# Kernel tuning notes

Hardware: AMD Instinct MI355X
Metric: run time of the kernel (lower is better)

## Reference

```python
import jax, jax.numpy as jnp
import numpy as np
from jax import lax

TAU = 1.0  # registered buffer, default 1.0 -> Q_tau = +inf -> clamp is a no-op
EPS = 1e-5
SQRT2 = float(np.sqrt(2.0))

# sign with straight-through estimator (weights): grad = identity
@jax.custom_vjp
def sign_w(w):
    return jnp.sign(w)
def _sign_w_fwd(w):
    return jnp.sign(w), None
def _sign_w_bwd(_, g):
    return (g,)
sign_w.defvjp(_sign_w_fwd, _sign_w_bwd)

@jax.custom_vjp
def sign_a(x):
    return jnp.sign(x)
def _sign_a_fwd(x):
    return jnp.sign(x), x
def _sign_a_bwd(x, g):
    return (jnp.maximum(2.0 - jnp.abs(2.0 * x), 0.0) * g,)
sign_a.defvjp(_sign_a_fwd, _sign_a_bwd)

def binarize_conv2d(a, w, alpha, stride=1):
    # weight standardization (torch.var is unbiased -> ddof=1)
    w0 = w - jnp.mean(w, axis=(1, 2, 3), keepdims=True)
    var = jnp.var(w0, axis=(1, 2, 3), keepdims=True, ddof=1)
    w1 = w0 * (2.0 * SQRT2) / jnp.sqrt(var + EPS)
    EW = jnp.mean(jnp.abs(w1))
    Q_tau = lax.stop_gradient(-EW * jnp.log(2.0 - 2.0 * TAU))  # +inf for tau=1
    w2 = jnp.clip(w1, -Q_tau, Q_tau)
    bw = sign_w(w2)
    ba = sign_a(a)  # eval mode: a0 = a (no per-sample var normalization)
    out = lax.conv_general_dilated(
        ba, bw, window_strides=(stride, stride), padding=((1, 1), (1, 1)),
        dimension_numbers=('NCHW', 'OIHW', 'NCHW'))
    return out * alpha[None]  # alpha: [C_out,1,1] -> broadcast over N,H,W

def bn_eval(x, gamma, beta, mean, var):
    scale = (gamma / jnp.sqrt(var + EPS)).reshape(1, -1, 1, 1)
    shift = (beta - mean * gamma / jnp.sqrt(var + EPS)).reshape(1, -1, 1, 1)
    return x * scale + shift

def hardtanh(x):
    return jnp.clip(x, -1.0, 1.0)

def setup_inputs() -> dict:
    key = jax.random.key(0)
    ks = jax.random.split(key, 13)
    N, C, H, W = 64, 256, 32, 32
    return {
        'x': jax.random.normal(ks[0], (N, C, H, W), jnp.float32),
        'conv1_w': jax.random.normal(ks[1], (C, C, 3, 3), jnp.float32) * 0.05,
        'alpha1': jax.random.uniform(ks[2], (C, 1, 1), jnp.float32),
        'bn1_gamma': jax.random.uniform(ks[3], (C,), jnp.float32) + 0.5,
        'bn1_beta': jax.random.normal(ks[4], (C,), jnp.float32) * 0.1,
        'bn1_mean': jax.random.normal(ks[5], (C,), jnp.float32),
        'bn1_var': jax.random.uniform(ks[6], (C,), jnp.float32) + 0.5,
        'conv2_w': jax.random.normal(ks[7], (C, C, 3, 3), jnp.float32) * 0.05,
        'alpha2': jax.random.uniform(ks[8], (C, 1, 1), jnp.float32),
        'bn2_gamma': jax.random.uniform(ks[9], (C,), jnp.float32) + 0.5,
        'bn2_beta': jax.random.normal(ks[10], (C,), jnp.float32) * 0.1,
        'bn2_mean': jax.random.normal(ks[11], (C,), jnp.float32),
        'bn2_var': jax.random.uniform(ks[12], (C,), jnp.float32) + 0.5,
    }

def reference(x, conv1_w, alpha1, bn1_gamma, bn1_beta, bn1_mean, bn1_var,
              conv2_w, alpha2, bn2_gamma, bn2_beta, bn2_mean, bn2_var):
    out = hardtanh(bn_eval(binarize_conv2d(x, conv1_w, alpha1, stride=1),
                           bn1_gamma, bn1_beta, bn1_mean, bn1_var))
    out = bn_eval(binarize_conv2d(out, conv2_w, alpha2, stride=1),
                  bn2_gamma, bn2_beta, bn2_mean, bn2_var)
    out = out + x  # identity shortcut (stride=1, in_planes==planes)
    return hardtanh(out)
```

## Files before the change

kernel.cpp:

```cpp
#include <hip/hip_runtime.h>
#include <cstdint>
#include <cstddef>

using u32 = unsigned int;
using u64 = unsigned long long;

typedef int v4i  __attribute__((ext_vector_type(4)));
typedef int v16i __attribute__((ext_vector_type(16)));

#define EPSV 1e-5f

__global__ void prep_weights(const float* __restrict__ w1, const float* __restrict__ w2,
                             const float* __restrict__ a1, const float* __restrict__ g1,
                             const float* __restrict__ b1, const float* __restrict__ m1,
                             const float* __restrict__ v1,
                             const float* __restrict__ a2, const float* __restrict__ g2,
                             const float* __restrict__ b2, const float* __restrict__ m2,
                             const float* __restrict__ v2,
                             unsigned char* __restrict__ Wsgn, float4* __restrict__ SC4)
{
    const int co   = blockIdx.x;
    const int conv = blockIdx.y;
    const int c    = threadIdx.x;
    const float* w = conv ? w2 : w1;

    float wv[9];
    const float* wp = w + ((size_t)co * 256 + c) * 9;
    float s = 0.f;
#pragma unroll
    for (int p = 0; p < 9; ++p) { wv[p] = wp[p]; s += wv[p]; }

    __shared__ float red[256];
    red[c] = s;
    __syncthreads();
    for (int off = 128; off > 0; off >>= 1) {
        if (c < off) red[c] += red[c + off];
        __syncthreads();
    }
    const float mean = __fdiv_rn(red[0], 2304.0f);

    unsigned char* wrow = Wsgn + ((size_t)(conv * 256 + co) * 9) * 256;
#pragma unroll
    for (int p = 0; p < 9; ++p)
        wrow[p * 256 + c] = (wv[p] > mean) ? 0x01u : 0xFFu;

    if (c == 0) {
        const float alpha = conv ? a2[co] : a1[co];
        const float gamma = conv ? g2[co] : g1[co];
        const float beta  = conv ? b2[co] : b1[co];
        const float mu    = conv ? m2[co] : m1[co];
        const float var   = conv ? v2[co] : v1[co];
        const float sq    = __fsqrt_rn(__fadd_rn(var, EPSV));
        const float scale = __fdiv_rn(gamma, sq);
        const float shift = __fsub_rn(beta, __fdiv_rn(__fmul_rn(mu, gamma), sq));
        SC4[conv * 256 + co] = make_float4(alpha, scale, shift, 0.f);
    }
}

__global__ void build_bfrag(const unsigned char* __restrict__ Wsgn, uint4* __restrict__ Bf)
{
    const int f    = blockIdx.x;
    const int lane = threadIdx.x;
    const int conv = f / 576;
    const int rem  = f % 576;
    const int g    = rem / 72;
    const int p    = (rem % 72) / 8;
    const int cb   = rem % 8;
    const int co   = g * 32 + (lane & 31);
    const unsigned char* src = Wsgn + ((size_t)(conv * 256 + co) * 9 + p) * 256
                                    + cb * 32 + (lane >> 5) * 16;
    Bf[(size_t)f * 64 + lane] = *(const uint4*)src;
}

__global__ void binarize_x(const float* __restrict__ x, u32* __restrict__ A1)
{
    const int n = blockIdx.x >> 3;
    const int j = blockIdx.x & 7;
    const int p = threadIdx.x;
    const float* xp = x + (((size_t)n * 256 + j * 32) * 1024) + p;
    u32 bits = 0;
#pragma unroll
    for (int k = 0; k < 32; ++k) {
        float v = xp[(size_t)k * 1024];
        bits |= (v > 0.f ? 1u : 0u) << k;
    }
    A1[((size_t)n * 1024 + p) * 8 + j] = bits;
}

__device__ __forceinline__ u32 expand4(u32 x)
{
    u32 r;
    r  = ((x & 1u) ? 0x00000001u : 0x000000FFu);
    r |= ((x & 2u) ? 0x00000100u : 0x0000FF00u);
    r |= ((x & 4u) ? 0x00010000u : 0x00FF0000u);
    r |= ((x & 8u) ? 0x01000000u : 0xFF000000u);
    return r;
}

__device__ __forceinline__ void glds16(const void* g, void* l)
{
    __builtin_amdgcn_global_load_lds(
        (const __attribute__((address_space(1))) void*)g,
        (__attribute__((address_space(3))) void*)l, 16, 0, 0);
}

template<int CONV>
__global__ __launch_bounds__(256, 2)
void conv_mfma(const u32* __restrict__ A_in, const v4i* __restrict__ Bf,
               const float4* __restrict__ SC4, const float* __restrict__ X,
               u32* __restrict__ A_out, float* __restrict__ OUT)
{
    const int n    = blockIdx.x >> 3;
    const int yq   = blockIdx.x & 7;
    const int y0   = yq * 4;
    const int tid  = threadIdx.x;
    const int wave = tid >> 6;
    const int lane = tid & 63;
    const int wm   = wave >> 1;
    const int wn   = wave & 1;
    const int col0 = lane & 31;

    __shared__ alignas(16) unsigned char lds[65536];

    const int fbias = (CONV == 2) ? 576 : 0;
    const char* bsrc0 = (const char*)Bf
        + (((size_t)(fbias + wave * 2 * 72)) << 10) + (size_t)lane * 16;

    glds16(bsrc0,              lds + wave * 2048);
    glds16(bsrc0 + (72 << 10), lds + wave * 2048 + 1024);

    for (int s = tid; s < 3072; s += 256) {
        const int xs   = s & 31;
        const int rest = s >> 5;
        const int r    = rest % 6;
        const int c16  = rest / 6;
        const int iy   = y0 - 1 + r;
        u32 d0 = 0, d1 = 0, d2 = 0, d3 = 0;
        if ((unsigned)iy < 32u) {
            const u32 wrd = A_in[((size_t)n * 1024 + iy * 32 + xs) * 8 + (c16 >> 1)];
            const u32 h = (wrd >> ((c16 & 1) * 16)) & 0xFFFFu;
            d0 = expand4(h);
            d1 = expand4(h >> 4);
            d2 = expand4(h >> 8);
            d3 = expand4(h >> 12);
        }
        *(uint4*)(lds + 16384 + (size_t)s * 16) = make_uint4(d0, d1, d2, d3);
    }
    __syncthreads();

    const v16i Z  = {0,0,0,0,0,0,0,0,0,0,0,0,0,0,0,0};
    const v4i  Z4 = {0,0,0,0};
    v16i c00 = Z, c01 = Z, c02 = Z, c03 = Z;
    v16i c10 = Z, c11 = Z, c12 = Z, c13 = Z;

    const u32 abase = 16384u + (u32)((lane >> 5) * 3072 + wm * 1024);
    const u32 bbase = (u32)(wn * 4096 + lane * 16);

#pragma unroll 1
    for (int k = 0; k < 72; ++k) {
        {
            int kn = k + 1; if (kn == 72) kn = 0;
            const char* s0 = bsrc0 + ((size_t)kn << 10);
            unsigned char* d = lds + (kn & 1) * 8192 + wave * 2048;
            glds16(s0, d);
            glds16(s0 + (72 << 10), d + 1024);
        }
        __builtin_amdgcn_sched_barrier(0);

        const int p  = k >> 3, cb = k & 7;
        const int dy = p / 3,  dx = p - dy * 3;
        int c = col0 + dx - 1; c = c < 0 ? 0 : (c > 31 ? 31 : c);
        const u32 ao = abase + (u32)(cb * 6144 + dy * 512 + c * 16);
        v4i a0 = *(const v4i*)(lds + ao);
        v4i a1 = *(const v4i*)(lds + ao + 512);
        const bool kill = (dx == 0 && col0 == 0) || (dx == 2 && col0 == 31);
        if (kill) { a0 = Z4; a1 = Z4; }

        const u32 bo = bbase + (u32)((k & 1) * 8192);
        const v4i b0 = *(const v4i*)(lds + bo);
        const v4i b1 = *(const v4i*)(lds + bo + 1024);
        const v4i b2 = *(const v4i*)(lds + bo + 2048);
        const v4i b3 = *(const v4i*)(lds + bo + 3072);

        __builtin_amdgcn_s_setprio(1);
        c00 = __builtin_amdgcn_mfma_i32_32x32x32_i8(a0, b0, c00, 0, 0, 0);
        c01 = __builtin_amdgcn_mfma_i32_32x32x32_i8(a0, b1, c01, 0, 0, 0);
        c02 = __builtin_amdgcn_mfma_i32_32x32x32_i8(a0, b2, c02, 0, 0, 0);
        c03 = __builtin_amdgcn_mfma_i32_32x32x32_i8(a0, b3, c03, 0, 0, 0);
        c10 = __builtin_amdgcn_mfma_i32_32x32x32_i8(a1, b0, c10, 0, 0, 0);
        c11 = __builtin_amdgcn_mfma_i32_32x32x32_i8(a1, b1, c11, 0, 0, 0);
        c12 = __builtin_amdgcn_mfma_i32_32x32x32_i8(a1, b2, c12, 0, 0, 0);
        c13 = __builtin_amdgcn_mfma_i32_32x32x32_i8(a1, b3, c13, 0, 0, 0);
        __builtin_amdgcn_s_setprio(0);

        __syncthreads();
    }

    const int bias2 = (CONV == 2) ? 256 : 0;
    const float4 sc0 = SC4[bias2 + (wn * 4 + 0) * 32 + col0];
    const float4 sc1 = SC4[bias2 + (wn * 4 + 1) * 32 + col0];
    const float4 sc2 = SC4[bias2 + (wn * 4 + 2) * 32 + col0];
    const float4 sc3 = SC4[bias2 + (wn * 4 + 3) * 32 + col0];

    if (CONV == 1) {
#define EP1(ACC, MI, NI, SC)                                                    \
        { _Pragma("unroll")                                                     \
          for (int reg = 0; reg < 16; ++reg) {                                  \
              const float t = __fadd_rn(__fmul_rn(__fmul_rn((float)ACC[reg],    \
                                        SC.x), SC.y), SC.z);                    \
              const u64 m = __ballot(t > 0.f);                                  \
              if (lane == 0) {                                                  \
                  const int x = (reg & 3) + 8 * (reg >> 2);                     \
                  const int row = y0 + 2 * wm + (MI);                           \
                  const size_t pb = (size_t)n * 1024 + row * 32 + x;            \
                  A_out[pb * 8 + (wn * 4 + (NI))]       = (u32)m;               \
                  A_out[(pb + 4) * 8 + (wn * 4 + (NI))] = (u32)(m >> 32);       \
              } } }
        EP1(c00, 0, 0, sc0)  EP1(c01, 0, 1, sc1)
        EP1(c02, 0, 2, sc2)  EP1(c03, 0, 3, sc3)
        EP1(c10, 1, 0, sc0)  EP1(c11, 1, 1, sc1)
        EP1(c12, 1, 2, sc2)  EP1(c13, 1, 3, sc3)
#undef EP1
    } else {
        __syncthreads();
        float* ep = (float*)lds;
#define EP2PASS(C0, C1, C2, C3, R)                                              \
        { if (wm == ((R) >> 1)) {                                               \
            _Pragma("unroll")                                                   \
            for (int reg = 0; reg < 16; ++reg) {                                \
                const int x = (reg & 3) + 8 * (reg >> 2) + 4 * (lane >> 5);     \
                ep[x * 257 + (wn * 4 + 0) * 32 + col0] =                        \
                    __fadd_rn(__fmul_rn(__fmul_rn((float)C0[reg], sc0.x),       \
                                        sc0.y), sc0.z);                         \
                ep[x * 257 + (wn * 4 + 1) * 32 + col0] =                        \
                    __fadd_rn(__fmul_rn(__fmul_rn((float)C1[reg], sc1.x),       \
                                        sc1.y), sc1.z);                         \
                ep[x * 257 + (wn * 4 + 2) * 32 + col0] =                        \
                    __fadd_rn(__fmul_rn(__fmul_rn((float)C2[reg], sc2.x),       \
                                        sc2.y), sc2.z);                         \
                ep[x * 257 + (wn * 4 + 3) * 32 + col0] =                        \
                    __fadd_rn(__fmul_rn(__fmul_rn((float)C3[reg], sc3.x),       \
                                        sc3.y), sc3.z);                         \
            } }                                                                 \
          __syncthreads();                                                      \
          {                                                                     \
              const int co = tid;                                               \
              const size_t gb = ((size_t)(n * 256 + co)) * 1024                 \
                              + (y0 + (R)) * 32;                                \
              _Pragma("unroll")                                                 \
              for (int x4 = 0; x4 < 32; x4 += 4) {                              \
                  float4 r;                                                     \
                  r.x = ep[(x4 + 0) * 257 + co];                                \
                  r.y = ep[(x4 + 1) * 257 + co];                                \
                  r.z = ep[(x4 + 2) * 257 + co];                                \
                  r.w = ep[(x4 + 3) * 257 + co];                                \
                  const float4 xv = *(const float4*)(X + gb + x4);              \
                  r.x = fminf(1.f, fmaxf(-1.f, __fadd_rn(r.x, xv.x)));          \
                  r.y = fminf(1.f, fmaxf(-1.f, __fadd_rn(r.y, xv.y)));          \
                  r.z = fminf(1.f, fmaxf(-1.f, __fadd_rn(r.z, xv.z)));          \
                  r.w = fminf(1.f, fmaxf(-1.f, __fadd_rn(r.w, xv.w)));          \
                  *(float4*)(OUT + gb + x4) = r;                                \
              }                                                                 \
          }                                                                     \
          __syncthreads(); }
        EP2PASS(c00, c01, c02, c03, 0)
        EP2PASS(c10, c11, c12, c13, 1)
        EP2PASS(c00, c01, c02, c03, 2)
        EP2PASS(c10, c11, c12, c13, 3)
#undef EP2PASS
    }
}

extern "C" void kernel_launch(void* const* d_in, const int* in_sizes, int n_in,
                              void* d_out, int out_size, void* d_ws, size_t ws_size,
                              hipStream_t stream)
{
    const float* x   = (const float*)d_in[0];
    const float* w1  = (const float*)d_in[1];
    const float* al1 = (const float*)d_in[2];
    const float* g1  = (const float*)d_in[3];
    const float* b1  = (const float*)d_in[4];
    const float* m1  = (const float*)d_in[5];
    const float* v1  = (const float*)d_in[6];
    const float* w2  = (const float*)d_in[7];
    const float* al2 = (const float*)d_in[8];
    const float* g2  = (const float*)d_in[9];
    const float* b2  = (const float*)d_in[10];
    const float* m2  = (const float*)d_in[11];
    const float* v2  = (const float*)d_in[12];
    float* out = (float*)d_out;

    char* ws = (char*)d_ws;
    float4*        SC4  = (float4*)(ws);
    unsigned char* Wsgn = (unsigned char*)(ws + (64u << 10));
    uint4*         Bf   = (uint4*)(ws + (2u << 20));
    u32*           A1   = (u32*)(ws + (4u << 20));
    u32*           A2   = (u32*)(ws + (6u << 20));
    (void)ws_size; (void)in_sizes; (void)n_in; (void)out_size;

    prep_weights<<<dim3(256, 2), 256, 0, stream>>>(w1, w2, al1, g1, b1, m1, v1,
                                                   al2, g2, b2, m2, v2, Wsgn, SC4);
    build_bfrag<<<dim3(1152), 64, 0, stream>>>(Wsgn, Bf);
    binarize_x<<<dim3(512), 1024, 0, stream>>>(x, A1);
    conv_mfma<1><<<dim3(512), 256, 0, stream>>>(A1, (const v4i*)Bf, SC4,
                                                nullptr, A2, nullptr);
    conv_mfma<2><<<dim3(512), 256, 0, stream>>>(A2, (const v4i*)Bf, SC4,
                                                x, nullptr, out);
}
```

Baseline: 139.3 us.

## Give each wave private weight slices, drop per-step block barriers

Each wave now covers all 4 output rows and its own 64 output channels, instead of a 2x2 wave grid that shared weight tiles through LDS. Weight tiles go into a per-wave 4-slot ring buffer, prefetched 3 steps ahead with global_load_lds. The per-k __syncthreads is replaced by an explicit s_waitcnt vmcnt. This removes block-wide barriers from the inner loop, but each wave now loads twice as many A fragments per step, and LDS grows to 80KB, which may limit the launch_bounds target of 2 blocks per CU.

```diff
diff --git a/kernel.cpp b/kernel.cpp
--- a/kernel.cpp
+++ b/kernel.cpp
@@ -116,18 +116,21 @@
     const int tid  = threadIdx.x;
     const int wave = tid >> 6;
     const int lane = tid & 63;
-    const int wm   = wave >> 1;
-    const int wn   = wave & 1;
     const int col0 = lane & 31;
 
-    __shared__ alignas(16) unsigned char lds[65536];
+    __shared__ alignas(16) unsigned char lds[81920];
 
     const int fbias = (CONV == 2) ? 576 : 0;
-    const char* bsrc0 = (const char*)Bf
-        + (((size_t)(fbias + wave * 2 * 72)) << 10) + (size_t)lane * 16;
-
-    glds16(bsrc0,              lds + wave * 2048);
-    glds16(bsrc0 + (72 << 10), lds + wave * 2048 + 1024);
+    const int g0 = wave * 2;
+    const char* bsrc0 = (const char*)Bf + (((size_t)(fbias + g0 * 72)) << 10)
+                        + (size_t)lane * 16;
+    unsigned char* bslot = lds + 49152 + wave * 8192;
+
+#pragma unroll
+    for (int i = 0; i < 3; ++i) {
+        glds16(bsrc0 + ((size_t)i << 10), bslot + i * 2048);
+        glds16(bsrc0 + ((size_t)i << 10) + 73728, bslot + i * 2048 + 1024);
+    }
 
     for (int s = tid; s < 3072; s += 256) {
         const int xs   = s & 31;
@@ -144,66 +147,68 @@
             d2 = expand4(h >> 8);
             d3 = expand4(h >> 12);
         }
-        *(uint4*)(lds + 16384 + (size_t)s * 16) = make_uint4(d0, d1, d2, d3);
+        *(uint4*)(lds + (size_t)s * 16) = make_uint4(d0, d1, d2, d3);
     }
     __syncthreads();
 
     const v16i Z  = {0,0,0,0,0,0,0,0,0,0,0,0,0,0,0,0};
     const v4i  Z4 = {0,0,0,0};
-    v16i c00 = Z, c01 = Z, c02 = Z, c03 = Z;
-    v16i c10 = Z, c11 = Z, c12 = Z, c13 = Z;
-
-    const u32 abase = 16384u + (u32)((lane >> 5) * 3072 + wm * 1024);
-    const u32 bbase = (u32)(wn * 4096 + lane * 16);
+    v16i c0a = Z, c0b = Z;
+    v16i c1a = Z, c1b = Z;
+    v16i c2a = Z, c2b = Z;
+    v16i c3a = Z, c3b = Z;
+
+    const u32 bb = 49152u + (u32)(wave * 8192 + lane * 16);
 
 #pragma unroll 1
     for (int k = 0; k < 72; ++k) {
         {
-            int kn = k + 1; if (kn == 72) kn = 0;
-            const char* s0 = bsrc0 + ((size_t)kn << 10);
-            unsigned char* d = lds + (kn & 1) * 8192 + wave * 2048;
+            const int kf  = k + 3;
+            const int kfm = (kf >= 72) ? kf - 72 : kf;
+            const char* s0 = bsrc0 + ((size_t)kfm << 10);
+            unsigned char* d = bslot + (kf & 3) * 2048;
             glds16(s0, d);
-            glds16(s0 + (72 << 10), d + 1024);
+            glds16(s0 + 73728, d + 1024);
         }
         __builtin_amdgcn_sched_barrier(0);
 
         const int p  = k >> 3, cb = k & 7;
         const int dy = p / 3,  dx = p - dy * 3;
         int c = col0 + dx - 1; c = c < 0 ? 0 : (c > 31 ? 31 : c);
-        const u32 ao = abase + (u32)(cb * 6144 + dy * 512 + c * 16);
+        const u32 ao = (u32)((lane >> 5) * 3072 + cb * 6144 + dy * 512 + c * 16);
         v4i a0 = *(const v4i*)(lds + ao);
         v4i a1 = *(const v4i*)(lds + ao + 512);
-        const bool kill = (dx == 0 && col0 == 0) || (dx == 2 && col0 == 31);
-        if (kill) { a0 = Z4; a1 = Z4; }
-
-        const u32 bo = bbase + (u32)((k & 1) * 8192);
+        v4i a2 = *(const v4i*)(lds + ao + 1024);
+        v4i a3 = *(const v4i*)(lds + ao + 1536);
+        if ((dx == 0 && col0 == 0) || (dx == 2 && col0 == 31)) {
+            a0 = Z4; a1 = Z4; a2 = Z4; a3 = Z4;
+        }
+
+        asm volatile("s_waitcnt vmcnt(6)" ::: "memory");
+        __builtin_amdgcn_sched_barrier(0);
+
+        const u32 bo = bb + (u32)((k & 3) * 2048);
         const v4i b0 = *(const v4i*)(lds + bo);
         const v4i b1 = *(const v4i*)(lds + bo + 1024);
-        const v4i b2 = *(const v4i*)(lds + bo + 2048);
-        const v4i b3 = *(const v4i*)(lds + bo + 3072);
 
         __builtin_amdgcn_s_setprio(1);
-        c00 = __builtin_amdgcn_mfma_i32_32x32x32_i8(a0, b0, c00, 0, 0, 0);
-        c01 = __builtin_amdgcn_mfma_i32_32x32x32_i8(a0, b1, c01, 0, 0, 0);
-        c02 = __builtin_amdgcn_mfma_i32_32x32x32_i8(a0, b2, c02, 0, 0, 0);
-        c03 = __builtin_amdgcn_mfma_i32_32x32x32_i8(a0, b3, c03, 0, 0, 0);
-        c10 = __builtin_amdgcn_mfma_i32_32x32x32_i8(a1, b0, c10, 0, 0, 0);
-        c11 = __builtin_amdgcn_mfma_i32_32x32x32_i8(a1, b1, c11, 0, 0, 0);
-        c12 = __builtin_amdgcn_mfma_i32_32x32x32_i8(a1, b2, c12, 0, 0, 0);
-        c13 = __builtin_amdgcn_mfma_i32_32x32x32_i8(a1, b3, c13, 0, 0, 0);
+        c0a = __builtin_amdgcn_mfma_i32_32x32x32_i8(a0, b0, c0a, 0, 0, 0);
+        c0b = __builtin_amdgcn_mfma_i32_32x32x32_i8(a0, b1, c0b, 0, 0, 0);
+        c1a = __builtin_amdgcn_mfma_i32_32x32x32_i8(a1, b0, c1a, 0, 0, 0);
+        c1b = __builtin_amdgcn_mfma_i32_32x32x32_i8(a1, b1, c1b, 0, 0, 0);
+        c2a = __builtin_amdgcn_mfma_i32_32x32x32_i8(a2, b0, c2a, 0, 0, 0);
+        c2b = __builtin_amdgcn_mfma_i32_32x32x32_i8(a2, b1, c2b, 0, 0, 0);
+        c3a = __builtin_amdgcn_mfma_i32_32x32x32_i8(a3, b0, c3a, 0, 0, 0);
+        c3b = __builtin_amdgcn_mfma_i32_32x32x32_i8(a3, b1, c3b, 0, 0, 0);
         __builtin_amdgcn_s_setprio(0);
-
-        __syncthreads();
     }
 
     const int bias2 = (CONV == 2) ? 256 : 0;
-    const float4 sc0 = SC4[bias2 + (wn * 4 + 0) * 32 + col0];
-    const float4 sc1 = SC4[bias2 + (wn * 4 + 1) * 32 + col0];
-    const float4 sc2 = SC4[bias2 + (wn * 4 + 2) * 32 + col0];
-    const float4 sc3 = SC4[bias2 + (wn * 4 + 3) * 32 + col0];
+    const float4 scA = SC4[bias2 + (g0 + 0) * 32 + col0];
+    const float4 scB = SC4[bias2 + (g0 + 1) * 32 + col0];
 
     if (CONV == 1) {
-#define EP1(ACC, MI, NI, SC)                                                    \
+#define EP1(ACC, R, G, SC)                                                      \
         { _Pragma("unroll")                                                     \
           for (int reg = 0; reg < 16; ++reg) {                                  \
               const float t = __fadd_rn(__fmul_rn(__fmul_rn((float)ACC[reg],    \
@@ -211,37 +216,29 @@
               const u64 m = __ballot(t > 0.f);                                  \
               if (lane == 0) {                                                  \
                   const int x = (reg & 3) + 8 * (reg >> 2);                     \
-                  const int row = y0 + 2 * wm + (MI);                           \
-                  const size_t pb = (size_t)n * 1024 + row * 32 + x;            \
-                  A_out[pb * 8 + (wn * 4 + (NI))]       = (u32)m;               \
-                  A_out[(pb + 4) * 8 + (wn * 4 + (NI))] = (u32)(m >> 32);       \
+                  const size_t pb = (size_t)n * 1024 + (y0 + (R)) * 32 + x;     \
+                  A_out[pb * 8 + (G)]       = (u32)m;                           \
+                  A_out[(pb + 4) * 8 + (G)] = (u32)(m >> 32);                   \
               } } }
-        EP1(c00, 0, 0, sc0)  EP1(c01, 0, 1, sc1)
-        EP1(c02, 0, 2, sc2)  EP1(c03, 0, 3, sc3)
-        EP1(c10, 1, 0, sc0)  EP1(c11, 1, 1, sc1)
-        EP1(c12, 1, 2, sc2)  EP1(c13, 1, 3, sc3)
+        EP1(c0a, 0, g0, scA)      EP1(c0b, 0, g0 + 1, scB)
+        EP1(c1a, 1, g0, scA)      EP1(c1b, 1, g0 + 1, scB)
+        EP1(c2a, 2, g0, scA)      EP1(c2b, 2, g0 + 1, scB)
+        EP1(c3a, 3, g0, scA)      EP1(c3b, 3, g0 + 1, scB)
 #undef EP1
     } else {
         __syncthreads();
         float* ep = (float*)lds;
-#define EP2PASS(C0, C1, C2, C3, R)                                              \
-        { if (wm == ((R) >> 1)) {                                               \
-            _Pragma("unroll")                                                   \
-            for (int reg = 0; reg < 16; ++reg) {                                \
-                const int x = (reg & 3) + 8 * (reg >> 2) + 4 * (lane >> 5);     \
-                ep[x * 257 + (wn * 4 + 0) * 32 + col0] =                        \
-                    __fadd_rn(__fmul_rn(__fmul_rn((float)C0[reg], sc0.x),       \
-                                        sc0.y), sc0.z);                         \
-                ep[x * 257 + (wn * 4 + 1) * 32 + col0] =                        \
-                    __fadd_rn(__fmul_rn(__fmul_rn((float)C1[reg], sc1.x),       \
-                                        sc1.y), sc1.z);                         \
-                ep[x * 257 + (wn * 4 + 2) * 32 + col0] =                        \
-                    __fadd_rn(__fmul_rn(__fmul_rn((float)C2[reg], sc2.x),       \
-                                        sc2.y), sc2.z);                         \
-                ep[x * 257 + (wn * 4 + 3) * 32 + col0] =                        \
-                    __fadd_rn(__fmul_rn(__fmul_rn((float)C3[reg], sc3.x),       \
-                                        sc3.y), sc3.z);                         \
-            } }                                                                 \
+#define EP2PASS(CA, CB, R)                                                      \
+        { _Pragma("unroll")                                                     \
+          for (int reg = 0; reg < 16; ++reg) {                                  \
+              const int x = (reg & 3) + 8 * (reg >> 2) + 4 * (lane >> 5);       \
+              ep[x * 257 + (g0 + 0) * 32 + col0] =                              \
+                  __fadd_rn(__fmul_rn(__fmul_rn((float)CA[reg], scA.x),         \
+                                      scA.y), scA.z);                           \
+              ep[x * 257 + (g0 + 1) * 32 + col0] =                              \
+                  __fadd_rn(__fmul_rn(__fmul_rn((float)CB[reg], scB.x),         \
+                                      scB.y), scB.z);                           \
+          }                                                                     \
           __syncthreads();                                                      \
           {                                                                     \
               const int co = tid;                                               \
@@ -249,24 +246,24 @@
                               + (y0 + (R)) * 32;                                \
               _Pragma("unroll")                                                 \
               for (int x4 = 0; x4 < 32; x4 += 4) {                              \
-                  float4 r;                                                     \
-                  r.x = ep[(x4 + 0) * 257 + co];                                \
-                  r.y = ep[(x4 + 1) * 257 + co];                                \
-                  r.z = ep[(x4 + 2) * 257 + co];                                \
-                  r.w = ep[(x4 + 3) * 257 + co];                                \
+                  float4 rr;                                                    \
+                  rr.x = ep[(x4 + 0) * 257 + co];                               \
+                  rr.y = ep[(x4 + 1) * 257 + co];                               \
+                  rr.z = ep[(x4 + 2) * 257 + co];                               \
+                  rr.w = ep[(x4 + 3) * 257 + co];                               \
                   const float4 xv = *(const float4*)(X + gb + x4);              \
-                  r.x = fminf(1.f, fmaxf(-1.f, __fadd_rn(r.x, xv.x)));          \
-                  r.y = fminf(1.f, fmaxf(-1.f, __fadd_rn(r.y, xv.y)));          \
-                  r.z = fminf(1.f, fmaxf(-1.f, __fadd_rn(r.z, xv.z)));          \
-                  r.w = fminf(1.f, fmaxf(-1.f, __fadd_rn(r.w, xv.w)));          \
-                  *(float4*)(OUT + gb + x4) = r;                                \
+                  rr.x = fminf(1.f, fmaxf(-1.f, __fadd_rn(rr.x, xv.x)));        \
+                  rr.y = fminf(1.f, fmaxf(-1.f, __fadd_rn(rr.y, xv.y)));        \
+                  rr.z = fminf(1.f, fmaxf(-1.f, __fadd_rn(rr.z, xv.z)));        \
+                  rr.w = fminf(1.f, fmaxf(-1.f, __fadd_rn(rr.w, xv.w)));        \
+                  *(float4*)(OUT + gb + x4) = rr;                               \
               }                                                                 \
           }                                                                     \
           __syncthreads(); }
-        EP2PASS(c00, c01, c02, c03, 0)
-        EP2PASS(c10, c11, c12, c13, 1)
-        EP2PASS(c00, c01, c02, c03, 2)
-        EP2PASS(c10, c11, c12, c13, 3)
+        EP2PASS(c0a, c0b, 0)
+        EP2PASS(c1a, c1b, 1)
+        EP2PASS(c2a, c2b, 2)
+        EP2PASS(c3a, c3b, 3)
 #undef EP2PASS
     }
 }
```

Result: no change. 138.6 us (-0.5%).
